# Performance work log

Hardware: AMD Instinct MI355X
Metric: run time of the kernel (lower is better)

Reference implementation:

```python
import jax, jax.numpy as jnp
import numpy as np

UNITS = 1024
OUT_STEPS = 200
SEQ_LEN = 5
NUM_FEATURES = 1
BATCH = 4096


def _lstm_cell(x, h, c, kernel, recurrent_kernel, bias):
    # Keras LSTMCell: z = x@K + h@R + b, gates in order i, f, g(candidate), o
    z = x @ kernel + h @ recurrent_kernel + bias  # [B, 4U]
    i, f, g, o = jnp.split(z, 4, axis=-1)
    i = jax.nn.sigmoid(i)
    f = jax.nn.sigmoid(f)
    g = jnp.tanh(g)
    o = jax.nn.sigmoid(o)
    c_new = f * c + i * g
    h_new = o * jnp.tanh(c_new)
    return h_new, c_new


def setup_inputs() -> dict:
    key = jax.random.key(0)
    ks = jax.random.split(key, 8)
    s = 0.05  # modest init scale to keep gates unsaturated
    return {
        "inputs": jax.random.normal(ks[0], (BATCH, SEQ_LEN, NUM_FEATURES), jnp.float32),
        "kernel": jax.random.normal(ks[1], (NUM_FEATURES, 4 * UNITS), jnp.float32) * s,
        "recurrent_kernel": jax.random.normal(ks[2], (UNITS, 4 * UNITS), jnp.float32) * s,
        "bias": jax.random.normal(ks[3], (4 * UNITS,), jnp.float32) * s,
        "w1": jax.random.normal(ks[4], (UNITS, NUM_FEATURES), jnp.float32) * s,
        "b1": jax.random.normal(ks[5], (NUM_FEATURES,), jnp.float32) * s,
        "w2": jax.random.normal(ks[6], (NUM_FEATURES, NUM_FEATURES), jnp.float32) * s,
        "b2": jax.random.normal(ks[7], (NUM_FEATURES,), jnp.float32) * s,
    }


def reference(inputs, kernel, recurrent_kernel, bias, w1, b1, w2, b2):
    B = inputs.shape[0]
    h0 = jnp.zeros((B, UNITS), inputs.dtype)
    c0 = jnp.zeros((B, UNITS), inputs.dtype)

    # warmup: run LSTM over the input sequence (lax.scan over time)
    def warm_step(carry, x_t):
        h, c = carry
        h, c = _lstm_cell(x_t, h, c, kernel, recurrent_kernel, bias)
        return (h, c), None

    (h, c), _ = jax.lax.scan(warm_step, (h0, c0), jnp.swapaxes(inputs, 0, 1))
    pred0 = jax.nn.relu(h @ w1 + b1)  # first prediction: dense1 only (per warmup())

    def dec_step(carry, _):
        pred, h, c = carry
        h, c = _lstm_cell(pred, h, c, kernel, recurrent_kernel, bias)
        x = jax.nn.relu(h @ w1 + b1)
        pred = x @ w2 + b2
        return (pred, h, c), pred

    _, preds = jax.lax.scan(dec_step, (pred0, h, c), None, length=OUT_STEPS - 1)
    # preds: [T-1, B, F] -> stack with pred0 and transpose to [B, T, F]
    all_preds = jnp.concatenate([pred0[None], preds], axis=0)
    return jnp.transpose(all_preds, (1, 0, 2))
```

## Files before the change

### kernel.cpp

```cpp
#include <hip/hip_runtime.h>
#include <hip/hip_bf16.h>
#include <stdint.h>
#include <stddef.h>

#define B_SZ   4096
#define U_SZ   1024
#define K_SZ   1024
#define SEQ    5
#define TSTEPS 200

#define TM  128
#define TNP 128
#define BK  64

typedef __bf16 bf16_t;
typedef __bf16 bf16x8 __attribute__((ext_vector_type(8)));
typedef float  f32x4  __attribute__((ext_vector_type(4)));

#define AS1 __attribute__((address_space(1)))
#define AS3 __attribute__((address_space(3)))

__device__ __forceinline__ void load_lds16(const void* g, void* l) {
    __builtin_amdgcn_global_load_lds((const AS1 unsigned int*)g,
                                     (AS3 unsigned int*)l, 16, 0, 0);
}

__device__ __forceinline__ float fsig(float x) {
    return 1.0f / (1.0f + __expf(-x));
}
__device__ __forceinline__ float ftanh(float x) {
    x = fminf(fmaxf(x, -15.0f), 15.0f);
    float e = __expf(2.0f * x);
    return (e - 1.0f) / (e + 1.0f);
}

__global__ void pack_R(const float* __restrict__ R, bf16_t* __restrict__ Rp) {
    int idx = blockIdx.x * 256 + threadIdx.x;
    int kk = idx & 63;
    int c  = (idx >> 6) & 127;
    int kb = (idx >> 13) & 15;
    int ub = idx >> 17;
    int g  = (c >> 4) & 3;
    int wc = c >> 6;
    int cl = c & 15;
    int n  = g * 1024 + ub * 32 + wc * 16 + cl;
    int k  = kb * 64 + kk;
    Rp[idx] = (bf16_t)R[(size_t)k * 4096 + n];
}

__global__ __launch_bounds__(256, 2)
void lstm_step(const bf16_t* __restrict__ hin,
               bf16_t* __restrict__ hout,
               float* __restrict__ cst,
               const bf16_t* __restrict__ Rp,
               const float* __restrict__ Wx,
               const float* __restrict__ bias,
               const float* __restrict__ xsrc, int xstride)
{
    __shared__ __align__(16) bf16_t lsA[TM * BK];
    __shared__ __align__(16) bf16_t lsB[TNP * BK];
    __shared__ float lsX[TM];

    const int tid  = threadIdx.x;
    const int wave = tid >> 6;
    const int lane = tid & 63;
    const int mb   = blockIdx.x;
    const int ub   = blockIdx.y;

    if (tid < TM) lsX[tid] = xsrc[(size_t)(mb * TM + tid) * xstride];

    f32x4 acc[4][4] = {};

    const bf16_t* Apanel = hin + (size_t)mb * TM * K_SZ;
    const bf16_t* Bpanel = Rp + (size_t)ub * 16 * (TNP * BK);

    const int rbase = (wave >> 1) * 64;
    const int cbase = (wave & 1) * 64;
    const int l15   = lane & 15;

    for (int kb = 0; kb < K_SZ / BK; ++kb) {
        #pragma unroll
        for (int i = 0; i < 4; ++i) {
            int chunk = wave * 4 + i;
            int m  = chunk * 8 + (lane >> 3);
            int kk = (lane & 7) * 8;
            const bf16_t* g = Apanel + (size_t)m * K_SZ + kb * BK + kk;
            load_lds16(g, &lsA[chunk * 512]);
        }
        const bf16_t* Bp = Bpanel + kb * (TNP * BK);
        #pragma unroll
        for (int i = 0; i < 4; ++i) {
            int chunk = wave * 4 + i;
            const bf16_t* g = Bp + chunk * 512 + lane * 8;
            load_lds16(g, &lsB[chunk * 512]);
        }
        __syncthreads();

        #pragma unroll
        for (int kh = 0; kh < 2; ++kh) {
            int ko = kh * 32 + ((lane >> 4) << 3);
            bf16x8 af[4], bfr[4];
            #pragma unroll
            for (int mi = 0; mi < 4; ++mi)
                af[mi] = *(const bf16x8*)&lsA[(rbase + mi * 16 + l15) * BK + ko];
            #pragma unroll
            for (int ni = 0; ni < 4; ++ni)
                bfr[ni] = *(const bf16x8*)&lsB[(cbase + ni * 16 + l15) * BK + ko];
            #pragma unroll
            for (int mi = 0; mi < 4; ++mi)
                #pragma unroll
                for (int ni = 0; ni < 4; ++ni)
                    acc[mi][ni] = __builtin_amdgcn_mfma_f32_16x16x32_bf16(
                        af[mi], bfr[ni], acc[mi][ni], 0, 0, 0);
        }
        __syncthreads();
    }

    const int wc = wave & 1;
    const int u  = ub * 32 + wc * 16 + l15;

    const float bi = bias[u],        wi = Wx[u];
    const float bf = bias[1024 + u], wf = Wx[1024 + u];
    const float bg = bias[2048 + u], wg = Wx[2048 + u];
    const float bo = bias[3072 + u], wo = Wx[3072 + u];
    const int rquad = (lane >> 4) << 2;

    #pragma unroll
    for (int mi = 0; mi < 4; ++mi) {
        int rlocal = rbase + mi * 16 + rquad;
        #pragma unroll
        for (int r = 0; r < 4; ++r) {
            int    brow = mb * TM + rlocal + r;
            float  xv   = lsX[rlocal + r];
            float zi = acc[mi][0][r] + bi + xv * wi;
            float zf = acc[mi][1][r] + bf + xv * wf;
            float zg = acc[mi][2][r] + bg + xv * wg;
            float zo = acc[mi][3][r] + bo + xv * wo;
            float ig = fsig(zi);
            float fg = fsig(zf);
            float gg = ftanh(zg);
            float og = fsig(zo);
            size_t off = (size_t)brow * U_SZ + u;
            float cn = fg * cst[off] + ig * gg;
            cst[off]  = cn;
            hout[off] = (bf16_t)(og * ftanh(cn));
        }
    }
}

__global__ __launch_bounds__(256)
void pred_step(const bf16_t* __restrict__ h, const float* __restrict__ w1,
               const float* __restrict__ b1, const float* __restrict__ w2,
               const float* __restrict__ b2, float* __restrict__ pred,
               float* __restrict__ out, int t, int mode)
{
    int b   = blockIdx.x;
    int tid = threadIdx.x;
    const bf16_t* hr = h + (size_t)b * U_SZ;
    float s = 0.f;
    #pragma unroll
    for (int j = 0; j < 4; ++j) {
        int idx = tid + j * 256;
        s += (float)hr[idx] * w1[idx];
    }
    #pragma unroll
    for (int off = 32; off > 0; off >>= 1)
        s += __shfl_down(s, off, 64);
    __shared__ float red[4];
    if ((tid & 63) == 0) red[tid >> 6] = s;
    __syncthreads();
    if (tid == 0) {
        float x1 = red[0] + red[1] + red[2] + red[3] + b1[0];
        x1 = fmaxf(x1, 0.f);
        float p = mode ? (x1 * w2[0] + b2[0]) : x1;
        pred[b] = p;
        out[(size_t)b * TSTEPS + t] = p;
    }
}

extern "C" void kernel_launch(void* const* d_in, const int* in_sizes, int n_in,
                              void* d_out, int out_size, void* d_ws, size_t ws_size,
                              hipStream_t stream) {
    const float* inputs = (const float*)d_in[0];
    const float* Wx     = (const float*)d_in[1];
    const float* R      = (const float*)d_in[2];
    const float* bias   = (const float*)d_in[3];
    const float* w1     = (const float*)d_in[4];
    const float* b1     = (const float*)d_in[5];
    const float* w2     = (const float*)d_in[6];
    const float* b2     = (const float*)d_in[7];
    float* out = (float*)d_out;

    char* ws = (char*)d_ws;
    const size_t RP_BYTES = (size_t)32 * 16 * 128 * 64 * 2;
    const size_t H_BYTES  = (size_t)B_SZ * U_SZ * 2;
    const size_t C_BYTES  = (size_t)B_SZ * U_SZ * 4;
    bf16_t* Rp   = (bf16_t*)ws;                 ws += RP_BYTES;
    bf16_t* h0   = (bf16_t*)ws;                 ws += H_BYTES;
    bf16_t* h1   = (bf16_t*)ws;                 ws += H_BYTES;
    float*  cbuf = (float*)ws;                  ws += C_BYTES;
    float*  pred = (float*)ws;                  ws += (size_t)B_SZ * 4;
    bf16_t* hb[2] = {h0, h1};

    hipMemsetAsync(h0, 0, H_BYTES, stream);
    hipMemsetAsync(cbuf, 0, C_BYTES, stream);

    pack_R<<<16384, 256, 0, stream>>>(R, Rp);

    dim3 grid(B_SZ / TM, U_SZ / 32);
    int cur = 0;
    for (int t = 0; t < SEQ; ++t) {
        lstm_step<<<grid, 256, 0, stream>>>(hb[cur], hb[1 - cur], cbuf, Rp, Wx,
                                            bias, inputs + t, SEQ);
        cur ^= 1;
    }
    pred_step<<<B_SZ, 256, 0, stream>>>(hb[cur], w1, b1, w2, b2, pred, out, 0, 0);
    for (int t = 1; t < TSTEPS; ++t) {
        lstm_step<<<grid, 256, 0, stream>>>(hb[cur], hb[1 - cur], cbuf, Rp, Wx,
                                            bias, pred, 1);
        cur ^= 1;
        pred_step<<<B_SZ, 256, 0, stream>>>(hb[cur], w1, b1, w2, b2, pred, out, t, 1);
    }
}
```

Measured before the change: 10.33 ms.

## Fuse prediction head into LSTM step via atomic partial dot products

Removes the separate per-step pred_step kernel by having each LSTM tile compute h·w1 partial sums in its epilogue and atomically add them into a triple-buffered row accumulator. The next step's kernel finishes relu/dense2, writes the output and zeroes the stale buffer. Each block now computes two unit groups (a 128x256 output tile), reusing the loaded A tile across twice as many columns, on a 16x32 grid. This halves the launch count and avoids re-reading h for the prediction. The costs are more accumulators per thread, more LDS, float atomics that make summation order nondeterministic, and one fewer block per unit slice.

```diff
diff --git a/kernel.cpp b/kernel.cpp
--- a/kernel.cpp
+++ b/kernel.cpp
@@ -5,13 +5,9 @@
 
 #define B_SZ   4096
 #define U_SZ   1024
-#define K_SZ   1024
 #define SEQ    5
 #define TSTEPS 200
-
-#define TM  128
-#define TNP 128
-#define BK  64
+#define STEPS  204
 
 typedef __bf16 bf16_t;
 typedef __bf16 bf16x8 __attribute__((ext_vector_type(8)));
@@ -20,10 +16,9 @@
 #define AS1 __attribute__((address_space(1)))
 #define AS3 __attribute__((address_space(3)))
 
-__device__ __forceinline__ void load_lds16(const void* g, void* l) {
-    __builtin_amdgcn_global_load_lds((const AS1 unsigned int*)g,
-                                     (AS3 unsigned int*)l, 16, 0, 0);
-}
+#define LOAD_LDS16(gp, lp) \
+    __builtin_amdgcn_global_load_lds((const AS1 unsigned int*)(gp), \
+                                     (AS3 unsigned int*)(lp), 16, 0, 0)
 
 __device__ __forceinline__ float fsig(float x) {
     return 1.0f / (1.0f + __expf(-x));
@@ -55,127 +50,153 @@
                const bf16_t* __restrict__ Rp,
                const float* __restrict__ Wx,
                const float* __restrict__ bias,
-               const float* __restrict__ xsrc, int xstride)
+               const float* __restrict__ w1,
+               const float* __restrict__ b1,
+               const float* __restrict__ w2,
+               const float* __restrict__ b2,
+               const float* __restrict__ inputs,
+               float* __restrict__ praw,
+               float* __restrict__ out,
+               int t)
 {
-    __shared__ __align__(16) bf16_t lsA[TM * BK];
-    __shared__ __align__(16) bf16_t lsB[TNP * BK];
-    __shared__ float lsX[TM];
+    __shared__ __align__(16) bf16_t lsA[128 * 64];
+    __shared__ __align__(16) bf16_t lsB[2][128 * 64];
+    __shared__ float lsX[128];
 
     const int tid  = threadIdx.x;
     const int wave = tid >> 6;
     const int lane = tid & 63;
-    const int mb   = blockIdx.x;
-    const int ub   = blockIdx.y;
-
-    if (tid < TM) lsX[tid] = xsrc[(size_t)(mb * TM + tid) * xstride];
-
-    f32x4 acc[4][4] = {};
-
-    const bf16_t* Apanel = hin + (size_t)mb * TM * K_SZ;
-    const bf16_t* Bpanel = Rp + (size_t)ub * 16 * (TNP * BK);
-
+    const int p    = blockIdx.x;
+    const int G    = blockIdx.y;
+    const int l15  = lane & 15;
+    const int quad = lane >> 4;
     const int rbase = (wave >> 1) * 64;
-    const int cbase = (wave & 1) * 64;
-    const int l15   = lane & 15;
-
-    for (int kb = 0; kb < K_SZ / BK; ++kb) {
+    const int wc    = wave & 1;
+
+    float*       pr_acc  = praw + (size_t)(t % 3) * B_SZ;
+    const float* pr_read = praw + (size_t)((t + 2) % 3) * B_SZ;
+    float*       pr_zero = praw + (size_t)((t + 1) % 3) * B_SZ;
+
+    if (tid < 128) {
+        int row = G * 128 + tid;
+        float x;
+        if (t < SEQ) {
+            x = inputs[row * SEQ + t];
+        } else {
+            float x1 = fmaxf(pr_read[row] + b1[0], 0.f);
+            x = (t == SEQ) ? x1 : x1 * w2[0] + b2[0];
+            if (p == 0) out[(size_t)row * TSTEPS + (t - SEQ)] = x;
+        }
+        lsX[tid] = x;
+        if (p == 0) pr_zero[row] = 0.f;
+    }
+
+    f32x4 acc[2][4][4] = {};
+    const bf16_t* Ap  = hin + (size_t)G * 128 * U_SZ;
+    const bf16_t* Bp0 = Rp + (size_t)(2 * p) * 131072;
+    const bf16_t* Bp1 = Bp0 + 131072;
+
+    for (int kb = 0; kb < 16; ++kb) {
         #pragma unroll
         for (int i = 0; i < 4; ++i) {
             int chunk = wave * 4 + i;
             int m  = chunk * 8 + (lane >> 3);
             int kk = (lane & 7) * 8;
-            const bf16_t* g = Apanel + (size_t)m * K_SZ + kb * BK + kk;
-            load_lds16(g, &lsA[chunk * 512]);
-        }
-        const bf16_t* Bp = Bpanel + kb * (TNP * BK);
+            LOAD_LDS16(Ap + (size_t)m * U_SZ + kb * 64 + kk, &lsA[chunk * 512]);
+        }
         #pragma unroll
         for (int i = 0; i < 4; ++i) {
             int chunk = wave * 4 + i;
-            const bf16_t* g = Bp + chunk * 512 + lane * 8;
-            load_lds16(g, &lsB[chunk * 512]);
+            LOAD_LDS16(Bp0 + (size_t)kb * 8192 + chunk * 512 + lane * 8,
+                       &lsB[0][chunk * 512]);
+            LOAD_LDS16(Bp1 + (size_t)kb * 8192 + chunk * 512 + lane * 8,
+                       &lsB[1][chunk * 512]);
         }
         __syncthreads();
 
         #pragma unroll
         for (int kh = 0; kh < 2; ++kh) {
-            int ko = kh * 32 + ((lane >> 4) << 3);
-            bf16x8 af[4], bfr[4];
+            int ko = kh * 32 + quad * 8;
+            bf16x8 af[4];
             #pragma unroll
             for (int mi = 0; mi < 4; ++mi)
-                af[mi] = *(const bf16x8*)&lsA[(rbase + mi * 16 + l15) * BK + ko];
+                af[mi] = *(const bf16x8*)&lsA[(rbase + mi * 16 + l15) * 64 + ko];
             #pragma unroll
-            for (int ni = 0; ni < 4; ++ni)
-                bfr[ni] = *(const bf16x8*)&lsB[(cbase + ni * 16 + l15) * BK + ko];
-            #pragma unroll
-            for (int mi = 0; mi < 4; ++mi)
+            for (int T = 0; T < 2; ++T) {
+                bf16x8 bfr[4];
                 #pragma unroll
                 for (int ni = 0; ni < 4; ++ni)
-                    acc[mi][ni] = __builtin_amdgcn_mfma_f32_16x16x32_bf16(
-                        af[mi], bfr[ni], acc[mi][ni], 0, 0, 0);
+                    bfr[ni] = *(const bf16x8*)
+                        &lsB[T][(wc * 64 + ni * 16 + l15) * 64 + ko];
+                #pragma unroll
+                for (int mi = 0; mi < 4; ++mi)
+                    #pragma unroll
+                    for (int ni = 0; ni < 4; ++ni)
+                        acc[T][mi][ni] = __builtin_amdgcn_mfma_f32_16x16x32_bf16(
+                            af[mi], bfr[ni], acc[T][mi][ni], 0, 0, 0);
+            }
         }
         __syncthreads();
     }
 
-    const int wc = wave & 1;
-    const int u  = ub * 32 + wc * 16 + l15;
-
-    const float bi = bias[u],        wi = Wx[u];
-    const float bf = bias[1024 + u], wf = Wx[1024 + u];
-    const float bg = bias[2048 + u], wg = Wx[2048 + u];
-    const float bo = bias[3072 + u], wo = Wx[3072 + u];
-    const int rquad = (lane >> 4) << 2;
+    int uu[2];
+    uu[0] = (2 * p) * 32 + wc * 16 + l15;
+    uu[1] = uu[0] + 32;
+    float g_b[2][4], g_w[2][4], w1u[2];
+    #pragma unroll
+    for (int T = 0; T < 2; ++T) {
+        #pragma unroll
+        for (int g = 0; g < 4; ++g) {
+            g_b[T][g] = bias[g * 1024 + uu[T]];
+            g_w[T][g] = Wx[g * 1024 + uu[T]];
+        }
+        w1u[T] = w1[uu[T]];
+    }
+    const bool do_pred = (t >= SEQ - 1);
 
     #pragma unroll
     for (int mi = 0; mi < 4; ++mi) {
-        int rlocal = rbase + mi * 16 + rquad;
         #pragma unroll
         for (int r = 0; r < 4; ++r) {
-            int    brow = mb * TM + rlocal + r;
-            float  xv   = lsX[rlocal + r];
-            float zi = acc[mi][0][r] + bi + xv * wi;
-            float zf = acc[mi][1][r] + bf + xv * wf;
-            float zg = acc[mi][2][r] + bg + xv * wg;
-            float zo = acc[mi][3][r] + bo + xv * wo;
-            float ig = fsig(zi);
-            float fg = fsig(zf);
-            float gg = ftanh(zg);
-            float og = fsig(zo);
-            size_t off = (size_t)brow * U_SZ + u;
-            float cn = fg * cst[off] + ig * gg;
-            cst[off]  = cn;
-            hout[off] = (bf16_t)(og * ftanh(cn));
-        }
-    }
-}
-
-__global__ __launch_bounds__(256)
-void pred_step(const bf16_t* __restrict__ h, const float* __restrict__ w1,
-               const float* __restrict__ b1, const float* __restrict__ w2,
-               const float* __restrict__ b2, float* __restrict__ pred,
-               float* __restrict__ out, int t, int mode)
+            int rl   = rbase + mi * 16 + quad * 4 + r;
+            int brow = G * 128 + rl;
+            float xv = lsX[rl];
+            float ps = 0.f;
+            #pragma unroll
+            for (int T = 0; T < 2; ++T) {
+                float zi = acc[T][mi][0][r] + g_b[T][0] + xv * g_w[T][0];
+                float zf = acc[T][mi][1][r] + g_b[T][1] + xv * g_w[T][1];
+                float zg = acc[T][mi][2][r] + g_b[T][2] + xv * g_w[T][2];
+                float zo = acc[T][mi][3][r] + g_b[T][3] + xv * g_w[T][3];
+                float ig = fsig(zi), fg = fsig(zf);
+                float gg = ftanh(zg), og = fsig(zo);
+                size_t off = (size_t)brow * U_SZ + uu[T];
+                float cn = fg * cst[off] + ig * gg;
+                cst[off] = cn;
+                float hv = og * ftanh(cn);
+                hout[off] = (bf16_t)hv;
+                ps += hv * w1u[T];
+            }
+            if (do_pred) {
+                ps += __shfl_xor(ps, 1);
+                ps += __shfl_xor(ps, 2);
+                ps += __shfl_xor(ps, 4);
+                ps += __shfl_xor(ps, 8);
+                if (l15 == 0) atomicAdd(&pr_acc[brow], ps);
+            }
+        }
+    }
+}
+
+__global__ void pred_final(const float* __restrict__ praw,
+                           const float* __restrict__ b1,
+                           const float* __restrict__ w2,
+                           const float* __restrict__ b2,
+                           float* __restrict__ out)
 {
-    int b   = blockIdx.x;
-    int tid = threadIdx.x;
-    const bf16_t* hr = h + (size_t)b * U_SZ;
-    float s = 0.f;
-    #pragma unroll
-    for (int j = 0; j < 4; ++j) {
-        int idx = tid + j * 256;
-        s += (float)hr[idx] * w1[idx];
-    }
-    #pragma unroll
-    for (int off = 32; off > 0; off >>= 1)
-        s += __shfl_down(s, off, 64);
-    __shared__ float red[4];
-    if ((tid & 63) == 0) red[tid >> 6] = s;
-    __syncthreads();
-    if (tid == 0) {
-        float x1 = red[0] + red[1] + red[2] + red[3] + b1[0];
-        x1 = fmaxf(x1, 0.f);
-        float p = mode ? (x1 * w2[0] + b2[0]) : x1;
-        pred[b] = p;
-        out[(size_t)b * TSTEPS + t] = p;
-    }
+    int row = blockIdx.x * 256 + threadIdx.x;
+    float x1 = fmaxf(praw[2 * B_SZ + row] + b1[0], 0.f);
+    out[(size_t)row * TSTEPS + 199] = x1 * w2[0] + b2[0];
 }
 
 extern "C" void kernel_launch(void* const* d_in, const int* in_sizes, int n_in,
@@ -192,33 +213,29 @@
     float* out = (float*)d_out;
 
     char* ws = (char*)d_ws;
-    const size_t RP_BYTES = (size_t)32 * 16 * 128 * 64 * 2;
+    const size_t RP_BYTES = (size_t)32 * 131072 * 2;
     const size_t H_BYTES  = (size_t)B_SZ * U_SZ * 2;
     const size_t C_BYTES  = (size_t)B_SZ * U_SZ * 4;
-    bf16_t* Rp   = (bf16_t*)ws;                 ws += RP_BYTES;
-    bf16_t* h0   = (bf16_t*)ws;                 ws += H_BYTES;
-    bf16_t* h1   = (bf16_t*)ws;                 ws += H_BYTES;
-    float*  cbuf = (float*)ws;                  ws += C_BYTES;
-    float*  pred = (float*)ws;                  ws += (size_t)B_SZ * 4;
+    bf16_t* Rp   = (bf16_t*)ws;                ws += RP_BYTES;
+    bf16_t* h0   = (bf16_t*)ws;                ws += H_BYTES;
+    bf16_t* h1   = (bf16_t*)ws;                ws += H_BYTES;
+    float*  cbuf = (float*)ws;                 ws += C_BYTES;
+    float*  praw = (float*)ws;                 ws += 3 * B_SZ * 4;
     bf16_t* hb[2] = {h0, h1};
 
     hipMemsetAsync(h0, 0, H_BYTES, stream);
     hipMemsetAsync(cbuf, 0, C_BYTES, stream);
+    hipMemsetAsync(praw, 0, 3 * B_SZ * 4, stream);
 
     pack_R<<<16384, 256, 0, stream>>>(R, Rp);
 
-    dim3 grid(B_SZ / TM, U_SZ / 32);
+    dim3 grid(16, 32);
     int cur = 0;
-    for (int t = 0; t < SEQ; ++t) {
-        lstm_step<<<grid, 256, 0, stream>>>(hb[cur], hb[1 - cur], cbuf, Rp, Wx,
-                                            bias, inputs + t, SEQ);
+    for (int t = 0; t < STEPS; ++t) {
+        lstm_step<<<grid, 256, 0, stream>>>(hb[cur], hb[1 - cur], cbuf, Rp,
+                                            Wx, bias, w1, b1, w2, b2,
+                                            inputs, praw, out, t);
         cur ^= 1;
     }
-    pred_step<<<B_SZ, 256, 0, stream>>>(hb[cur], w1, b1, w2, b2, pred, out, 0, 0);
-    for (int t = 1; t < TSTEPS; ++t) {
-        lstm_step<<<grid, 256, 0, stream>>>(hb[cur], hb[1 - cur], cbuf, Rp, Wx,
-                                            bias, pred, 1);
-        cur ^= 1;
-        pred_step<<<B_SZ, 256, 0, stream>>>(hb[cur], w1, b1, w2, b2, pred, out, t, 1);
-    }
-}
+    pred_final<<<16, 256, 0, stream>>>(praw, b1, w2, b2, out);
+}
```

Measured after the change: 10.06 ms. 2.6% less time.
